# Kernel tuning notes

Measured on AMD Instinct MI355X. Metric: run time of the kernel, lower is better.

## Reference

```python
import jax, jax.numpy as jnp
import numpy as np

K = 20  # hard-coded in DGCNN.__init__

def _pd_neg(x):
    # negative squared pairwise distance, [B,N,C] -> [B,N,N]
    inner = jnp.einsum('bnc,bmc->bnm', x, x)
    sq = jnp.sum(x * x, axis=-1)
    return 2.0 * inner - sq[:, :, None] - sq[:, None, :]

def _knn(x):
    return jax.lax.top_k(_pd_neg(x), K)[1]  # [B,N,K]

def _edge_feat(x, idx):
    # x: [B,N,C], idx: [B,N,K] -> [B,N,K,2C] = concat(central, neighbor-central)
    nb = jax.vmap(lambda p, i: p[i])(x, idx)
    c = x[:, :, None, :]
    return jnp.concatenate([jnp.broadcast_to(c, nb.shape), nb - c], axis=-1)

def _conv(x, w, b, act=True):
    # 1x1 Conv2d == per-point linear; BN at inference with init stats is identity
    y = jnp.einsum('...c,cd->...d', x, w) + b
    return jax.nn.relu(y) if act else y

def _forward(x, tw1, tb1, tw2, tb2, tw3, tb3, tfw1, tfb1, tfw2, tfb2, txw, txb,
             e1w1, e1b1, e1w2, e1b2, e2w1, e2b1, e2w2, e2b2, e3w1, e3b1,
             c1w, c1b, c2w, c2b, c3w, c3b, c4w, c4b):
    pts = x[:, :, :3]
    # spatial transform net on edge features of raw xyz
    ef = _edge_feat(pts, _knn(pts))                      # [B,N,K,6]
    t = _conv(_conv(ef, tw1, tb1), tw2, tb2)
    t = jnp.max(t, axis=2)                               # max over neighbors
    t = _conv(t, tw3, tb3)                               # [B,N,1024]
    t = jnp.max(t, axis=1)                               # global maxpool -> [B,1024]
    t = jax.nn.relu(t @ tfw1 + tfb1)
    t = jax.nn.relu(t @ tfw2 + tfb2)
    xf = (t @ txw + txb).reshape(-1, 3, 3)
    p = jnp.einsum('bnc,bcd->bnd', pts, xf)              # transformed points
    # EdgeConv 1
    ef = _edge_feat(p, _knn(p))                          # [B,N,K,6]
    x1 = jnp.max(_conv(_conv(ef, e1w1, e1b1), e1w2, e1b2), axis=2)   # [B,N,64]
    # EdgeConv 2
    ef = _edge_feat(x1, _knn(x1))                        # [B,N,K,128]
    x2 = jnp.max(_conv(_conv(ef, e2w1, e2b1), e2w2, e2b2), axis=2)
    # EdgeConv 3
    ef = _edge_feat(x2, _knn(x2))
    x3 = jnp.max(_conv(ef, e3w1, e3b1), axis=2)
    # global feature + per-point head
    net = _conv(jnp.concatenate([x1, x2, x3], axis=-1), c1w, c1b)    # [B,N,1024]
    g = jnp.max(net, axis=1, keepdims=True)              # maxpool over all points
    g = jnp.broadcast_to(g, (g.shape[0], x1.shape[1], g.shape[2]))
    net = jnp.concatenate([g, x1, x2, x3], axis=-1)      # [B,N,1216]
    net = _conv(net, c2w, c2b)
    net = _conv(net, c3w, c3b)
    # dropout is identity at inference (training=False)
    return _conv(net, c4w, c4b, act=False)               # [B,N,num_classes]

def setup_inputs():
    keys = iter(jax.random.split(jax.random.key(0), 64))
    def w(*shape):
        return jax.random.normal(next(keys), shape, jnp.float32) / np.float32(np.sqrt(shape[0]))
    def b(n):
        return 0.01 * jax.random.normal(next(keys), (n,), jnp.float32)
    B, N, F = 4, 4096, 6
    d = dict(x=jax.random.normal(next(keys), (B, N, F), jnp.float32))
    d.update(tw1=w(6, 64), tb1=b(64), tw2=w(64, 128), tb2=b(128), tw3=w(128, 1024), tb3=b(1024),
             tfw1=w(1024, 512), tfb1=b(512), tfw2=w(512, 256), tfb2=b(256),
             txw=0.01 * w(256, 9), txb=jnp.eye(3, dtype=jnp.float32).reshape(9))
    d.update(e1w1=w(6, 64), e1b1=b(64), e1w2=w(64, 64), e1b2=b(64),
             e2w1=w(128, 64), e2b1=b(64), e2w2=w(64, 64), e2b2=b(64),
             e3w1=w(128, 64), e3b1=b(64))
    d.update(c1w=w(192, 1024), c1b=b(1024), c2w=w(1216, 512), c2b=b(512),
             c3w=w(512, 256), c3b=b(256), c4w=w(256, 2), c4b=b(2))
    return d

def reference(x, tw1, tb1, tw2, tb2, tw3, tb3, tfw1, tfb1, tfw2, tfb2, txw, txb,
              e1w1, e1b1, e1w2, e1b2, e2w1, e2b1, e2w2, e2b2, e3w1, e3b1,
              c1w, c1b, c2w, c2b, c3w, c3b, c4w, c4b):
    return _forward(x, tw1, tb1, tw2, tb2, tw3, tb3, tfw1, tfb1, tfw2, tfb2, txw, txb,
                    e1w1, e1b1, e1w2, e1b2, e2w1, e2b1, e2w2, e2b2, e3w1, e3b1,
                    c1w, c1b, c2w, c2b, c3w, c3b, c4w, c4b)
```

## Files before the change

kernel.cpp:

```cpp
#include <hip/hip_runtime.h>

#define Nn 4096
#define KK 20
#define BN 16384

typedef __attribute__((ext_vector_type(8))) short bf16x8;
typedef __attribute__((ext_vector_type(4))) float f32x4;

__device__ __forceinline__ unsigned short f2bf(float f) {
  unsigned int x = __float_as_uint(f);
  return (unsigned short)((x + 0x7fffu + ((x >> 16) & 1u)) >> 16);
}
__device__ __forceinline__ float bf2f(unsigned short u) {
  return __uint_as_float(((unsigned int)u) << 16);
}

__global__ void k_pts(const float* __restrict__ x, float* __restrict__ pts) {
  int i = blockIdx.x * 256 + threadIdx.x;
  if (i < BN * 3) {
    int pt = i / 3, c = i - 3 * pt;
    pts[i] = x[pt * 6 + c];
  }
}

__global__ void k_cvtT(const float* __restrict__ src, unsigned short* __restrict__ dst,
                       int N, int K, int ldn, int row0) {
  int i = blockIdx.x * 256 + threadIdx.x;
  if (i >= N * K) return;
  int n = i / K, k = i - n * K;
  dst[i] = f2bf(src[(size_t)(row0 + k) * ldn + n]);
}

__global__ void k_cvtT3(const float* __restrict__ src, unsigned short* __restrict__ h,
                        unsigned short* __restrict__ m, unsigned short* __restrict__ l,
                        int N, int K, int ldn) {
  int i = blockIdx.x * 256 + threadIdx.x;
  if (i >= N * K) return;
  int n = i / K, k = i - n * K;
  float x = src[(size_t)k * ldn + n];
  unsigned short hh = f2bf(x); float xh = bf2f(hh);
  unsigned short mm = f2bf(x - xh); float xm = bf2f(mm);
  unsigned short ll = f2bf(x - xh - xm);
  h[i] = hh; m[i] = mm; l[i] = ll;
}

__global__ void k_tv3(const float* __restrict__ part, const float* __restrict__ bias,
                      unsigned short* __restrict__ h, unsigned short* __restrict__ m,
                      unsigned short* __restrict__ l) {
  int i = blockIdx.x * 256 + threadIdx.x;
  if (i >= 16 * 1024) return;
  int row = i >> 10, col = i & 1023;
  float v = 0.f;
  if (row < 4) {
    float mx = -INFINITY;
#pragma unroll 8
    for (int s = 0; s < 32; ++s) mx = fmaxf(mx, part[((size_t)row * 32 + s) * 1024 + col]);
    v = fmaxf(mx + bias[col], 0.f);
  }
  unsigned short hh = f2bf(v); float xh = bf2f(hh);
  unsigned short mm = f2bf(v - xh); float xm = bf2f(mm);
  unsigned short ll = f2bf(v - xh - xm);
  h[i] = hh; m[i] = mm; l[i] = ll;
}

__global__ void k_pad3(const float* __restrict__ src, int rows, int cols,
                       unsigned short* __restrict__ h, unsigned short* __restrict__ m,
                       unsigned short* __restrict__ l) {
  int i = blockIdx.x * 256 + threadIdx.x;
  if (i >= 16 * cols) return;
  int row = i / cols, col = i - row * cols;
  float v = (row < rows) ? src[(size_t)row * cols + col] : 0.f;
  unsigned short hh = f2bf(v); float xh = bf2f(hh);
  unsigned short mm = f2bf(v - xh); float xm = bf2f(mm);
  unsigned short ll = f2bf(v - xh - xm);
  h[i] = hh; m[i] = mm; l[i] = ll;
}

template <int N, int K, int SEG>
__global__ __launch_bounds__(256) void k_gemmSK(const unsigned short* __restrict__ Ah,
                                                const unsigned short* __restrict__ Am,
                                                const unsigned short* __restrict__ Al,
                                                const unsigned short* __restrict__ Bh,
                                                const unsigned short* __restrict__ Bm,
                                                const unsigned short* __restrict__ Bl,
                                                float* __restrict__ partial) {
  constexpr int KSEG = K / SEG;
  constexpr int KS = KSEG / 32;
  int t = threadIdx.x;
  int wv = t >> 6, lane = t & 63;
  int quad = lane >> 4, l16 = lane & 15;
  int bx = blockIdx.x;
  int nb = bx / SEG, seg = bx - nb * SEG;
  int col = nb * 64 + wv * 16 + l16;
  int k0 = seg * KSEG;
  size_t wo = (size_t)col * K + k0 + quad * 8;
  size_t ao = (size_t)l16 * K + k0 + quad * 8;
  f32x4 acc = {0.f, 0.f, 0.f, 0.f};
#pragma unroll
  for (int s = 0; s < KS; ++s) {
    bf16x8 xh = *(const bf16x8*)(Ah + ao + s * 32);
    bf16x8 xm = *(const bf16x8*)(Am + ao + s * 32);
    bf16x8 xl = *(const bf16x8*)(Al + ao + s * 32);
    bf16x8 wh = *(const bf16x8*)(Bh + wo + s * 32);
    bf16x8 wm = *(const bf16x8*)(Bm + wo + s * 32);
    bf16x8 wl = *(const bf16x8*)(Bl + wo + s * 32);
    acc = __builtin_amdgcn_mfma_f32_16x16x32_bf16(xh, wh, acc, 0, 0, 0);
    acc = __builtin_amdgcn_mfma_f32_16x16x32_bf16(xh, wm, acc, 0, 0, 0);
    acc = __builtin_amdgcn_mfma_f32_16x16x32_bf16(xm, wh, acc, 0, 0, 0);
    acc = __builtin_amdgcn_mfma_f32_16x16x32_bf16(xh, wl, acc, 0, 0, 0);
    acc = __builtin_amdgcn_mfma_f32_16x16x32_bf16(xl, wh, acc, 0, 0, 0);
    acc = __builtin_amdgcn_mfma_f32_16x16x32_bf16(xm, wm, acc, 0, 0, 0);
  }
  if (quad == 0) {
#pragma unroll
    for (int r = 0; r < 4; ++r)
      partial[((size_t)seg * 4 + r) * N + col] = acc[r];
  }
}

__global__ void k_redS(const float* __restrict__ partial, const float* __restrict__ bias,
                       float* __restrict__ outp, int N, int SEG, int relu) {
  int i = blockIdx.x * 256 + threadIdx.x;
  if (i >= 4 * N) return;
  int r = i / N, c = i - r * N;
  float s = 0.f;
  for (int seg = 0; seg < SEG; ++seg) s += partial[((size_t)seg * 4 + r) * N + c];
  if (bias) s += bias[c];
  if (relu) s = fmaxf(s, 0.f);
  outp[(size_t)r * N + c] = s;
}

__global__ __launch_bounds__(256) void k_fc3p(const float* __restrict__ h2, const float* __restrict__ txw,
                                              const float* __restrict__ txb, const float* __restrict__ pts,
                                              float* __restrict__ p) {
  __shared__ float sh2[256];
  __shared__ float sxf[9];
  int t = threadIdx.x;
  int b = blockIdx.x;
  sh2[t] = h2[(size_t)b * 256 + t];
  __syncthreads();
  if (t < 9) {
    float acc = txb[t];
    for (int j = 0; j < 256; ++j) acc = fmaf(sh2[j], txw[j * 9 + t], acc);
    sxf[t] = acc;
  }
  __syncthreads();
  for (int n = t; n < Nn; n += 256) {
    const float* pr = pts + ((size_t)b * Nn + n) * 3;
    float a0 = pr[0], a1 = pr[1], a2 = pr[2];
    float* po = p + ((size_t)b * Nn + n) * 3;
#pragma unroll
    for (int d = 0; d < 3; ++d) po[d] = a0 * sxf[d] + a1 * sxf[3 + d] + a2 * sxf[6 + d];
  }
}

__device__ __forceinline__ float dist4(const float4* __restrict__ tile4, int c,
                                       float qx, float qy, float qz, float qsq) {
  float4 v = tile4[c];
  float dot = fmaf(qx, v.x, fmaf(qy, v.y, qz * v.z));
  return 2.0f * dot - qsq - v.w;
}

__global__ __launch_bounds__(1024) void k_knn3(const float* __restrict__ src, int* __restrict__ idx) {
  __shared__ float4 tile4[Nn];
  int t = threadIdx.x;
  int wave = t >> 6, lane = t & 63;
  int g = blockIdx.x * 16 + wave;
  int b = g >> 12, n = g & (Nn - 1);
  const float* base = src + (size_t)b * Nn * 3;
  for (int e = t; e < Nn; e += 1024) {
    float x = base[e * 3], y = base[e * 3 + 1], z = base[e * 3 + 2];
    tile4[e] = make_float4(x, y, z, fmaf(x, x, fmaf(y, y, z * z)));
  }
  __syncthreads();
  float4 q4 = tile4[n];
  float qx = q4.x, qy = q4.y, qz = q4.z, qsq = q4.w;
  float m1 = -INFINITY, m2 = -INFINITY, m3 = -INFINITY;
  int t1 = 0, t2 = 0, t3 = 0;
#pragma unroll 4
  for (int tt = 0; tt < 64; ++tt) {
    float dd = dist4(tile4, (tt << 6) + lane, qx, qy, qz, qsq);
    if (dd > m3) {
      if (dd > m1) { m3 = m2; t3 = t2; m2 = m1; t2 = t1; m1 = dd; t1 = tt; }
      else if (dd > m2) { m3 = m2; t3 = t2; m2 = dd; t2 = tt; }
      else { m3 = dd; t3 = tt; }
    }
  }
  unsigned long long removed = 0ull;
  int cnt = 3;
  int sel = 0;
#pragma unroll 1
  for (int k = 0; k < 20; ++k) {
    float v = m1; int ci = (t1 << 6) | lane;
    float mx = v;
#pragma unroll
    for (int off = 32; off; off >>= 1) mx = fmaxf(mx, __shfl_xor(mx, off, 64));
    int cand = (v == mx) ? ci : 0x7FFFFFFF;
#pragma unroll
    for (int off = 32; off; off >>= 1) cand = min(cand, __shfl_xor(cand, off, 64));
    if (k == lane) sel = cand;
    if (cand == ci) {
      removed |= 1ull << t1;
      if (cnt > 1) { m1 = m2; t1 = t2; m2 = m3; t2 = t3; --cnt; }
      else {
        m1 = -INFINITY; m2 = -INFINITY; m3 = -INFINITY; t1 = 0; t2 = 0; t3 = 0;
#pragma unroll 1
        for (int tt = 0; tt < 64; ++tt) {
          if ((removed >> tt) & 1ull) continue;
          float dd = dist4(tile4, (tt << 6) + lane, qx, qy, qz, qsq);
          if (dd > m3) {
            if (dd > m1) { m3 = m2; t3 = t2; m2 = m1; t2 = t1; m1 = dd; t1 = tt; }
            else if (dd > m2) { m3 = m2; t3 = t2; m2 = dd; t2 = tt; }
            else { m3 = dd; t3 = tt; }
          }
        }
        cnt = 3;
      }
    }
  }
  if (lane < 20) idx[(size_t)g * KK + lane] = sel;
}

__global__ void k_sqnorm(const float* __restrict__ src, float* __restrict__ out) {
  int g = blockIdx.x * 256 + threadIdx.x;
  if (g >= BN) return;
  const float4* r = (const float4*)(src + (size_t)g * 64);
  float s = 0.f;
#pragma unroll
  for (int j = 0; j < 16; ++j) { float4 v = r[j]; s += v.x * v.x + v.y * v.y + v.z * v.z + v.w * v.w; }
  out[g] = s;
}

__device__ __forceinline__ void topk_d3(const float (&d)[64], float m1, int t1, float m2, int t2,
                                        float m3, int t3, int lane, int* __restrict__ op) {
  unsigned long long removed = 0ull;
  int cnt = 3;
  int sel = 0;
#pragma unroll 1
  for (int k = 0; k < 20; ++k) {
    float v = m1; int ci = (t1 << 6) | lane;
    float mx = v;
#pragma unroll
    for (int off = 32; off; off >>= 1) mx = fmaxf(mx, __shfl_xor(mx, off, 64));
    int cand = (v == mx) ? ci : 0x7FFFFFFF;
#pragma unroll
    for (int off = 32; off; off >>= 1) cand = min(cand, __shfl_xor(cand, off, 64));
    if (k == lane) sel = cand;
    if (cand == ci) {
      removed |= 1ull << t1;
      if (cnt > 1) { m1 = m2; t1 = t2; m2 = m3; t2 = t3; --cnt; }
      else {
        m1 = -INFINITY; m2 = -INFINITY; m3 = -INFINITY; t1 = 0; t2 = 0; t3 = 0;
#pragma unroll
        for (int tt = 0; tt < 64; ++tt) {
          if (!((removed >> tt) & 1ull)) {
            float dv = d[tt];
            if (dv > m3) {
              if (dv > m1) { m3 = m2; t3 = t2; m2 = m1; t2 = t1; m1 = dv; t1 = tt; }
              else if (dv > m2) { m3 = m2; t3 = t2; m2 = dv; t2 = tt; }
              else { m3 = dv; t3 = tt; }
            }
          }
        }
        cnt = 3;
      }
    }
  }
  if (lane < 20) op[lane] = sel;
}

__global__ void __launch_bounds__(1024)
__attribute__((amdgpu_waves_per_eu(4, 4)))
k_dsel(const unsigned short* __restrict__ Xh,
       const unsigned short* __restrict__ Xm,
       const unsigned short* __restrict__ Xl,
       const float* __restrict__ sq,
       int* __restrict__ idx) {
  __shared__ float sD[16 * 1028];
  int t = threadIdx.x;
  int wave = t >> 6, lane = t & 63;
  int quad = lane >> 4, l16 = lane & 15;
  int blk = blockIdx.x;
  int b = blk >> 8, rs = blk & 255;
  int r0 = rs * 16;
  const size_t base = (size_t)b * Nn * 64;
  const float* sqb = sq + b * Nn;
  bf16x8 ah[2], am[2], al[2];
#pragma unroll
  for (int ks = 0; ks < 2; ++ks) {
    size_t ra = base + (size_t)(r0 + l16) * 64 + ks * 32 + quad * 8;
    ah[ks] = *(const bf16x8*)(Xh + ra);
    am[ks] = *(const bf16x8*)(Xm + ra);
    al[ks] = *(const bf16x8*)(Xl + ra);
  }
  float sqr[4];
#pragma unroll
  for (int r = 0; r < 4; ++r) sqr[r] = sqb[r0 + quad * 4 + r];
  float d[64];
  float m1 = -INFINITY, m2 = -INFINITY, m3 = -INFINITY;
  int t1 = 0, t2 = 0, t3 = 0;
#pragma unroll
  for (int ch = 0; ch < 4; ++ch) {
#pragma unroll
    for (int tt = 0; tt < 4; ++tt) {
      int cc = wave * 64 + tt * 16;
      int cb = ch * 1024 + cc;
      f32x4 acc = {0.f, 0.f, 0.f, 0.f};
#pragma unroll
      for (int ks = 0; ks < 2; ++ks) {
        size_t rb = base + (size_t)(cb + l16) * 64 + ks * 32 + quad * 8;
        bf16x8 bh = *(const bf16x8*)(Xh + rb);
        bf16x8 bm = *(const bf16x8*)(Xm + rb);
        bf16x8 bl = *(const bf16x8*)(Xl + rb);
        acc = __builtin_amdgcn_mfma_f32_16x16x32_bf16(ah[ks], bh, acc, 0, 0, 0);
        acc = __builtin_amdgcn_mfma_f32_16x16x32_bf16(ah[ks], bm, acc, 0, 0, 0);
        acc = __builtin_amdgcn_mfma_f32_16x16x32_bf16(am[ks], bh, acc, 0, 0, 0);
        acc = __builtin_amdgcn_mfma_f32_16x16x32_bf16(ah[ks], bl, acc, 0, 0, 0);
        acc = __builtin_amdgcn_mfma_f32_16x16x32_bf16(al[ks], bh, acc, 0, 0, 0);
        acc = __builtin_amdgcn_mfma_f32_16x16x32_bf16(am[ks], bm, acc, 0, 0, 0);
      }
      float sqc = sqb[cb + l16];
#pragma unroll
      for (int r = 0; r < 4; ++r)
        sD[(quad * 4 + r) * 1028 + cc + l16] = 2.0f * acc[r] - sqr[r] - sqc;
    }
    __syncthreads();
#pragma unroll
    for (int jj = 0; jj < 16; ++jj) {
      int tt = ch * 16 + jj;
      float dd = sD[wave * 1028 + jj * 64 + lane];
      d[tt] = dd;
      if (dd > m3) {
        if (dd > m1) { m3 = m2; t3 = t2; m2 = m1; t2 = t1; m1 = dd; t1 = tt; }
        else if (dd > m2) { m3 = m2; t3 = t2; m2 = dd; t2 = tt; }
        else { m3 = dd; t3 = tt; }
      }
    }
    __syncthreads();
  }
  topk_d3(d, m1, t1, m2, t2, m3, t3, lane, idx + (size_t)(b * Nn + r0 + wave) * KK);
}

__global__ __launch_bounds__(256) void k_uv3(const float* __restrict__ pts, const float* __restrict__ w1,
                                             const float* __restrict__ b1, float* __restrict__ uvb) {
  __shared__ float sw[384];
  __shared__ float sb[64];
  int t = threadIdx.x;
  for (int e = t; e < 384; e += 256) sw[e] = w1[e];
  if (t < 64) sb[t] = b1[t];
  __syncthreads();
  int pl = t >> 6, c = t & 63;
  int p = blockIdx.x * 4 + pl;
  const float* pr = pts + (size_t)p * 3;
  float x0 = pr[0], x1 = pr[1], x2 = pr[2];
  float wb0 = sw[192 + c], wb1 = sw[256 + c], wb2 = sw[320 + c];
  float v = x0 * wb0 + x1 * wb1 + x2 * wb2;
  float u = sb[c] + x0 * (sw[c] - wb0) + x1 * (sw[64 + c] - wb1) + x2 * (sw[128 + c] - wb2);
  uvb[(size_t)p * 128 + c] = u;
  uvb[(size_t)p * 128 + 64 + c] = v;
}

__global__ void k_prepD(const float* __restrict__ w1, float* __restrict__ Md) {
  int i = blockIdx.x * 256 + threadIdx.x;
  if (i >= 8192) return;
  int j = i >> 7, c = i & 127;
  Md[i] = (c < 64) ? (w1[j * 64 + c] - w1[(64 + j) * 64 + c]) : w1[(64 + j) * 64 + (c - 64)];
}

__global__ __launch_bounds__(256) void k_uv(const float* __restrict__ x2, const float* __restrict__ Md,
                                            const float* __restrict__ bias, float* __restrict__ uv) {
  __shared__ float sM[8192];
  __shared__ float sx[64 * 68];
  int t = threadIdx.x;
  for (int e = t; e < 8192; e += 256) sM[e] = Md[e];
  int p0 = blockIdx.x * 64;
  for (int e = t; e < 1024; e += 256) {
    int r = e >> 4, c4 = e & 15;
    *(float4*)(sx + r * 68 + c4 * 4) = *(const float4*)(x2 + (size_t)(p0 + r) * 64 + c4 * 4);
  }
  __syncthreads();
  int c = t & 127, rg = t >> 7;
  float badd = (c < 64) ? bias[c] : 0.f;
  float accv[32];
#pragma unroll
  for (int r = 0; r < 32; ++r) accv[r] = 0.f;
#pragma unroll
  for (int jc = 0; jc < 8; ++jc) {
    float mreg[8];
#pragma unroll
    for (int q = 0; q < 8; ++q) mreg[q] = sM[(jc * 8 + q) * 128 + c];
#pragma unroll
    for (int r = 0; r < 32; ++r) {
      const float* xr = sx + (rg * 32 + r) * 68 + jc * 8;
      float4 a = *(const float4*)xr, bb = *(const float4*)(xr + 4);
      float s = accv[r];
      s = fmaf(a.x, mreg[0], s); s = fmaf(a.y, mreg[1], s);
      s = fmaf(a.z, mreg[2], s); s = fmaf(a.w, mreg[3], s);
      s = fmaf(bb.x, mreg[4], s); s = fmaf(bb.y, mreg[5], s);
      s = fmaf(bb.z, mreg[6], s); s = fmaf(bb.w, mreg[7], s);
      accv[r] = s;
    }
  }
#pragma unroll
  for (int r = 0; r < 32; ++r)
    uv[(size_t)(p0 + rg * 32 + r) * 128 + c] = accv[r] + badd;
}

template <int NOUT, bool WRITEF, bool SPLIT3, bool CAT>
__global__ __launch_bounds__(256, 4) void k_econv(const float* __restrict__ uv,
                                                  const int* __restrict__ idx,
                                                  const unsigned short* __restrict__ W2h,
                                                  const unsigned short* __restrict__ W2m,
                                                  const unsigned short* __restrict__ W2l,
                                                  const float* __restrict__ b2,
                                                  float* __restrict__ outF,
                                                  unsigned short* __restrict__ oh,
                                                  unsigned short* __restrict__ om,
                                                  unsigned short* __restrict__ ol,
                                                  unsigned short* __restrict__ ocat,
                                                  int catoff) {
  __shared__ unsigned short y3[4][3][20 * 72];
  int t = threadIdx.x;
  int wv = t >> 6, lane = t & 63;
  int quad = lane >> 4, l16 = lane & 15;
  int p0 = blockIdx.x * 4;
  int p = p0 + wv;
  size_t nbase = (size_t)(p >> 12) * Nn;
  constexpr int CT = NOUT / 64;
  bf16x8 wfh[CT][2], wfm[CT][2], wfl[CT][2];
#pragma unroll
  for (int ct = 0; ct < CT; ++ct)
#pragma unroll
    for (int ks = 0; ks < 2; ++ks) {
      size_t wo = (size_t)(wv * (CT * 16) + ct * 16 + l16) * 64 + ks * 32 + quad * 8;
      wfh[ct][ks] = *(const bf16x8*)(W2h + wo);
      wfm[ct][ks] = *(const bf16x8*)(W2m + wo);
      wfl[ct][ks] = *(const bf16x8*)(W2l + wo);
    }
  const int* ip = idx + (size_t)p * KK;
  float u = uv[(size_t)p * 128 + lane];
  unsigned short* yh = y3[wv][0];
  unsigned short* ym = y3[wv][1];
  unsigned short* yl = y3[wv][2];
  float vv[20];
#pragma unroll
  for (int k = 0; k < 20; ++k) {
    int nb = ip[k];
    vv[k] = uv[(nbase + nb) * 128 + 64 + lane];
  }
#pragma unroll
  for (int k = 0; k < 20; ++k) {
    float y = fmaxf(u + vv[k], 0.f);
    unsigned short hh = f2bf(y); float fh = bf2f(hh);
    unsigned short mm = f2bf(y - fh); float fm = bf2f(mm);
    unsigned short ll = f2bf(y - fh - fm);
    yh[k * 72 + lane] = hh;
    ym[k * 72 + lane] = mm;
    yl[k * 72 + lane] = ll;
  }
  __syncthreads();
#pragma unroll 1
  for (int pp = 0; pp < 4; ++pp) {
    const unsigned short* ph0 = y3[pp][0];
    const unsigned short* pm0 = y3[pp][1];
    const unsigned short* pl0 = y3[pp][2];
    f32x4 acc[CT][2];
#pragma unroll
    for (int ct = 0; ct < CT; ++ct) {
      acc[ct][0] = (f32x4){0.f, 0.f, 0.f, 0.f};
      acc[ct][1] = (f32x4){0.f, 0.f, 0.f, 0.f};
    }
#pragma unroll
    for (int ks = 0; ks < 2; ++ks) {
      bf16x8 ah[2], am[2], al[2];
#pragma unroll
      for (int mt = 0; mt < 2; ++mt) {
        int row = mt * 16 + l16;
        int rr = (row < 20) ? row : 0;
        int aoff = rr * 72 + ks * 32 + quad * 8;
        ah[mt] = *(const bf16x8*)(ph0 + aoff);
        am[mt] = *(const bf16x8*)(pm0 + aoff);
        al[mt] = *(const bf16x8*)(pl0 + aoff);
      }
#pragma unroll
      for (int ct = 0; ct < CT; ++ct)
#pragma unroll
        for (int mt = 0; mt < 2; ++mt) {
          f32x4 a = acc[ct][mt];
          a = __builtin_amdgcn_mfma_f32_16x16x32_bf16(ah[mt], wfh[ct][ks], a, 0, 0, 0);
          a = __builtin_amdgcn_mfma_f32_16x16x32_bf16(ah[mt], wfm[ct][ks], a, 0, 0, 0);
          a = __builtin_amdgcn_mfma_f32_16x16x32_bf16(am[mt], wfh[ct][ks], a, 0, 0, 0);
          a = __builtin_amdgcn_mfma_f32_16x16x32_bf16(ah[mt], wfl[ct][ks], a, 0, 0, 0);
          a = __builtin_amdgcn_mfma_f32_16x16x32_bf16(al[mt], wfh[ct][ks], a, 0, 0, 0);
          a = __builtin_amdgcn_mfma_f32_16x16x32_bf16(am[mt], wfm[ct][ks], a, 0, 0, 0);
          acc[ct][mt] = a;
        }
    }
    int pt = p0 + pp;
#pragma unroll
    for (int ct = 0; ct < CT; ++ct) {
      int col = wv * (CT * 16) + ct * 16 + l16;
      float m0 = fmaxf(fmaxf(acc[ct][0][0], acc[ct][0][1]), fmaxf(acc[ct][0][2], acc[ct][0][3]));
      float m1v = (quad == 0)
                      ? fmaxf(fmaxf(acc[ct][1][0], acc[ct][1][1]), fmaxf(acc[ct][1][2], acc[ct][1][3]))
                      : -INFINITY;
      float m = fmaxf(m0, m1v);
      m = fmaxf(m, __shfl_xor(m, 16, 64));
      m = fmaxf(m, __shfl_xor(m, 32, 64));
      if (quad == 0) {
        float v = fmaxf(m + b2[col], 0.f);
        if (WRITEF) outF[(size_t)pt * NOUT + col] = v;
        if (SPLIT3) {
          unsigned short hh = f2bf(v); float fh = bf2f(hh);
          unsigned short mm2 = f2bf(v - fh); float fm = bf2f(mm2);
          unsigned short ll = f2bf(v - fh - fm);
          oh[(size_t)pt * NOUT + col] = hh;
          om[(size_t)pt * NOUT + col] = mm2;
          ol[(size_t)pt * NOUT + col] = ll;
        }
        if (CAT) ocat[(size_t)pt * 192 + catoff + col] = f2bf(v);
      }
    }
  }
}

__global__ __launch_bounds__(256) void k_gmax(const float* __restrict__ uv, const int* __restrict__ idx,
                                              unsigned short* __restrict__ ocat) {
  __shared__ int sidx[4][20];
  int t = threadIdx.x;
  int pl = t >> 6, c = t & 63;
  int p0 = blockIdx.x * 4;
  if (t < 80) sidx[t / 20][t % 20] = idx[(size_t)(p0 + t / 20) * KK + (t % 20)];
  __syncthreads();
  int p = p0 + pl;
  size_t nbase = (size_t)(p >> 12) * Nn;
  float u = uv[(size_t)p * 128 + c];
  float m = -INFINITY;
#pragma unroll
  for (int k = 0; k < 20; ++k) m = fmaxf(m, uv[(nbase + sidx[pl][k]) * 128 + 64 + c]);
  ocat[(size_t)p * 192 + 128 + c] = f2bf(fmaxf(u + m, 0.f));
}

template <int K>
__global__ __launch_bounds__(256) void k_mgemm(const unsigned short* __restrict__ A,
                                               const unsigned short* __restrict__ WT,
                                               float* __restrict__ outp) {
  constexpr int KS = K / 32;
  int t = threadIdx.x;
  int wv = t >> 6, lane = t & 63;
  int quad = lane >> 4, l16 = lane & 15;
  int blk = blockIdx.x;
  int b = blk >> 9, cb = (blk >> 5) & 15, ns = blk & 31;
  int n0 = cb * 64 + wv * 16;
  bf16x8 bfr[KS];
  const unsigned short* wrow = WT + (size_t)(n0 + l16) * K + quad * 8;
#pragma unroll
  for (int s = 0; s < KS; ++s) bfr[s] = *(const bf16x8*)(wrow + s * 32);
  const unsigned short* Ab = A + ((size_t)b * Nn + ns * 128 + l16) * K + quad * 8;
  float rmax = -INFINITY;
#pragma unroll 2
  for (int mt = 0; mt < 8; ++mt) {
    const unsigned short* ar = Ab + (size_t)mt * 16 * K;
    f32x4 acc = {0.f, 0.f, 0.f, 0.f};
#pragma unroll
    for (int s = 0; s < KS; ++s) {
      bf16x8 af = *(const bf16x8*)(ar + s * 32);
      acc = __builtin_amdgcn_mfma_f32_16x16x32_bf16(af, bfr[s], acc, 0, 0, 0);
    }
    rmax = fmaxf(rmax, fmaxf(fmaxf(acc[0], acc[1]), fmaxf(acc[2], acc[3])));
  }
  rmax = fmaxf(rmax, __shfl_xor(rmax, 16, 64));
  rmax = fmaxf(rmax, __shfl_xor(rmax, 32, 64));
  if (quad == 0) outp[((size_t)b * 32 + ns) * 1024 + n0 + l16] = rmax;
}

template <int K>
__global__ __launch_bounds__(256) void k_mgemm3s(const unsigned short* __restrict__ Ah,
                                                 const unsigned short* __restrict__ Am,
                                                 const unsigned short* __restrict__ Al,
                                                 const unsigned short* __restrict__ Bh,
                                                 const unsigned short* __restrict__ Bm,
                                                 const unsigned short* __restrict__ Bl,
                                                 float* __restrict__ outp) {
  constexpr int KS = K / 32;
  int t = threadIdx.x;
  int wv = t >> 6, lane = t & 63;
  int quad = lane >> 4, l16 = lane & 15;
  int blk = blockIdx.x;
  int b = blk >> 9, cb = (blk >> 5) & 15, ns = blk & 31;
  int n0 = cb * 64 + wv * 16;
  bf16x8 wh[KS], wm[KS], wl[KS];
  size_t wo = (size_t)(n0 + l16) * K + quad * 8;
#pragma unroll
  for (int s = 0; s < KS; ++s) {
    wh[s] = *(const bf16x8*)(Bh + wo + s * 32);
    wm[s] = *(const bf16x8*)(Bm + wo + s * 32);
    wl[s] = *(const bf16x8*)(Bl + wo + s * 32);
  }
  size_t ao = ((size_t)b * Nn + ns * 128 + l16) * K + quad * 8;
  float rmax = -INFINITY;
#pragma unroll 1
  for (int mt = 0; mt < 8; ++mt) {
    size_t ar = ao + (size_t)mt * 16 * K;
    f32x4 acc = {0.f, 0.f, 0.f, 0.f};
#pragma unroll
    for (int s = 0; s < KS; ++s) {
      bf16x8 xh = *(const bf16x8*)(Ah + ar + s * 32);
      bf16x8 xm = *(const bf16x8*)(Am + ar + s * 32);
      bf16x8 xl = *(const bf16x8*)(Al + ar + s * 32);
      acc = __builtin_amdgcn_mfma_f32_16x16x32_bf16(xh, wh[s], acc, 0, 0, 0);
      acc = __builtin_amdgcn_mfma_f32_16x16x32_bf16(xh, wm[s], acc, 0, 0, 0);
      acc = __builtin_amdgcn_mfma_f32_16x16x32_bf16(xm, wh[s], acc, 0, 0, 0);
      acc = __builtin_amdgcn_mfma_f32_16x16x32_bf16(xh, wl[s], acc, 0, 0, 0);
      acc = __builtin_amdgcn_mfma_f32_16x16x32_bf16(xl, wh[s], acc, 0, 0, 0);
      acc = __builtin_amdgcn_mfma_f32_16x16x32_bf16(xm, wm[s], acc, 0, 0, 0);
    }
    rmax = fmaxf(rmax, fmaxf(fmaxf(acc[0], acc[1]), fmaxf(acc[2], acc[3])));
  }
  rmax = fmaxf(rmax, __shfl_xor(rmax, 16, 64));
  rmax = fmaxf(rmax, __shfl_xor(rmax, 32, 64));
  if (quad == 0) outp[((size_t)b * 32 + ns) * 1024 + n0 + l16] = rmax;
}

__global__ __launch_bounds__(256) void k_final(const unsigned short* __restrict__ xcat,
                                               const float* __restrict__ gc,
                                               const float* __restrict__ c2b,
                                               const unsigned short* __restrict__ c2wT,
                                               const unsigned short* __restrict__ c3wT,
                                               const float* __restrict__ c3b,
                                               const float* __restrict__ c4w, const float* __restrict__ c4b,
                                               float* __restrict__ out) {
  __shared__ unsigned short z5[16 * 520];
  __shared__ float z2[16 * 260];
  int t = threadIdx.x;
  int wv = t >> 6, lane = t & 63;
  int quad = lane >> 4, l16 = lane & 15;
  int p0 = blockIdx.x * 16;
  int b = p0 >> 12;
  bf16x8 a1[6];
  const unsigned short* ar = xcat + (size_t)(p0 + l16) * 192 + quad * 8;
#pragma unroll
  for (int s = 0; s < 6; ++s) a1[s] = *(const bf16x8*)(ar + s * 32);
#pragma unroll 1
  for (int ntw = 0; ntw < 8; ++ntw) {
    int col = wv * 128 + ntw * 16 + l16;
    float bias = gc[(size_t)b * 512 + col] + c2b[col];
    f32x4 acc = {bias, bias, bias, bias};
    const unsigned short* wr = c2wT + (size_t)col * 192 + quad * 8;
#pragma unroll
    for (int s = 0; s < 6; ++s) {
      bf16x8 bfr = *(const bf16x8*)(wr + s * 32);
      acc = __builtin_amdgcn_mfma_f32_16x16x32_bf16(a1[s], bfr, acc, 0, 0, 0);
    }
#pragma unroll
    for (int r = 0; r < 4; ++r)
      z5[(quad * 4 + r) * 520 + col] = f2bf(fmaxf(acc[r], 0.f));
  }
  __syncthreads();
  bf16x8 a2[16];
#pragma unroll
  for (int s = 0; s < 16; ++s) a2[s] = *(const bf16x8*)(z5 + l16 * 520 + s * 32 + quad * 8);
#pragma unroll 1
  for (int ntw = 0; ntw < 4; ++ntw) {
    int col = wv * 64 + ntw * 16 + l16;
    float bias = c3b[col];
    f32x4 acc = {bias, bias, bias, bias};
    const unsigned short* wr = c3wT + (size_t)col * 512 + quad * 8;
#pragma unroll
    for (int s = 0; s < 16; ++s) {
      bf16x8 bfr = *(const bf16x8*)(wr + s * 32);
      acc = __builtin_amdgcn_mfma_f32_16x16x32_bf16(a2[s], bfr, acc, 0, 0, 0);
    }
#pragma unroll
    for (int r = 0; r < 4; ++r)
      z2[(quad * 4 + r) * 260 + col] = fmaxf(acc[r], 0.f);
  }
  __syncthreads();
  if (t < 32) {
    int m = t >> 1, e = t & 1;
    float acc = c4b[e];
    const float* zr = z2 + m * 260;
    for (int j = 0; j < 256; ++j) acc = fmaf(zr[j], c4w[j * 2 + e], acc);
    out[(size_t)(p0 + m) * 2 + e] = acc;
  }
}

extern "C" void kernel_launch(void* const* d_in, const int* in_sizes, int n_in,
                              void* d_out, int out_size, void* d_ws, size_t ws_size,
                              hipStream_t stream) {
  const float* xin = (const float*)d_in[0];
  const float* W[30];
  for (int i = 0; i < 30; ++i) W[i] = (const float*)d_in[i + 1];

  float* ws = (float*)d_ws;
  size_t off = 0;
  float* pts   = ws + off; off += (size_t)BN * 3;
  float* p     = ws + off; off += (size_t)BN * 3;
  int*   idx   = (int*)(ws + off); off += (size_t)BN * KK;
  float* sq    = ws + off; off += BN;
  float* dpart = ws + off; off += 4 * 32 * 1024;
  float* h1    = ws + off; off += 4 * 512;
  float* h2b   = ws + off; off += 4 * 256;
  float* x1    = ws + off; off += (size_t)BN * 64;
  float* x2    = ws + off; off += (size_t)BN * 64;
  float* gpart = ws + off; off += 4 * 32 * 1024;
  float* gc    = ws + off; off += 4 * 512;
  float* uvb   = ws + off; off += (size_t)BN * 128;
  float* partial = ws + off; off += 16 * 4 * 512;
  unsigned short* xcat = (unsigned short*)(ws + off); off += (size_t)BN * 96;
  unsigned short* c1wT = (unsigned short*)(ws + off); off += 98304;
  unsigned short* c2wT = (unsigned short*)(ws + off); off += 49152;
  unsigned short* c3wT = (unsigned short*)(ws + off); off += 65536;
  unsigned short* w3Th = (unsigned short*)(ws + off); off += 65536;
  unsigned short* w3Tm = (unsigned short*)(ws + off); off += 65536;
  unsigned short* w3Tl = (unsigned short*)(ws + off); off += 65536;
  unsigned short* tw2h = (unsigned short*)(ws + off); off += 4096;
  unsigned short* tw2m = (unsigned short*)(ws + off); off += 4096;
  unsigned short* tw2l = (unsigned short*)(ws + off); off += 4096;
  unsigned short* e1h  = (unsigned short*)(ws + off); off += 2048;
  unsigned short* e1m  = (unsigned short*)(ws + off); off += 2048;
  unsigned short* e1l  = (unsigned short*)(ws + off); off += 2048;
  unsigned short* e2h  = (unsigned short*)(ws + off); off += 2048;
  unsigned short* e2m  = (unsigned short*)(ws + off); off += 2048;
  unsigned short* e2l  = (unsigned short*)(ws + off); off += 2048;
  unsigned short* xsh  = (unsigned short*)(ws + off); off += 524288;
  unsigned short* xsm  = (unsigned short*)(ws + off); off += 524288;
  unsigned short* xsl  = (unsigned short*)(ws + off); off += 524288;
  float* MdC   = ws + off; off += 8192;
  float* MdD   = ws + off; off += 8192;
  unsigned short* fw1h = (unsigned short*)(ws + off); off += 262144;
  unsigned short* fw1m = (unsigned short*)(ws + off); off += 262144;
  unsigned short* fw1l = (unsigned short*)(ws + off); off += 262144;
  unsigned short* cw2h = (unsigned short*)(ws + off); off += 262144;
  unsigned short* cw2m = (unsigned short*)(ws + off); off += 262144;
  unsigned short* cw2l = (unsigned short*)(ws + off); off += 262144;
  unsigned short* fw2h = (unsigned short*)(ws + off); off += 65536;
  unsigned short* fw2m = (unsigned short*)(ws + off); off += 65536;
  unsigned short* fw2l = (unsigned short*)(ws + off); off += 65536;
  unsigned short* tvh  = (unsigned short*)(ws + off); off += 8192;
  unsigned short* tvm  = (unsigned short*)(ws + off); off += 8192;
  unsigned short* tvl  = (unsigned short*)(ws + off); off += 8192;
  unsigned short* h13h = (unsigned short*)(ws + off); off += 4096;
  unsigned short* h13m = (unsigned short*)(ws + off); off += 4096;
  unsigned short* h13l = (unsigned short*)(ws + off); off += 4096;
  float* Dbuf  = ws + off; off += (size_t)Nn * Nn;
  unsigned short* t3h = (unsigned short*)Dbuf;
  unsigned short* t3m = t3h + (size_t)BN * 128;
  unsigned short* t3l = t3m + (size_t)BN * 128;

  k_cvtT<<<dim3(768), dim3(256), 0, stream>>>(W[22], c1wT, 1024, 192, 1024, 0);
  k_cvtT<<<dim3(384), dim3(256), 0, stream>>>(W[24], c2wT, 512, 192, 512, 1024);
  k_cvtT<<<dim3(512), dim3(256), 0, stream>>>(W[26], c3wT, 256, 512, 256, 0);
  k_cvtT3<<<dim3(512), dim3(256), 0, stream>>>(W[4], w3Th, w3Tm, w3Tl, 1024, 128, 1024);
  k_cvtT3<<<dim3(32), dim3(256), 0, stream>>>(W[2], tw2h, tw2m, tw2l, 128, 64, 128);
  k_cvtT3<<<dim3(16), dim3(256), 0, stream>>>(W[14], e1h, e1m, e1l, 64, 64, 64);
  k_cvtT3<<<dim3(16), dim3(256), 0, stream>>>(W[18], e2h, e2m, e2l, 64, 64, 64);
  k_cvtT3<<<dim3(2048), dim3(256), 0, stream>>>(W[6], fw1h, fw1m, fw1l, 512, 1024, 512);
  k_cvtT3<<<dim3(2048), dim3(256), 0, stream>>>(W[24], cw2h, cw2m, cw2l, 512, 1024, 512);
  k_cvtT3<<<dim3(512), dim3(256), 0, stream>>>(W[8], fw2h, fw2m, fw2l, 256, 512, 256);
  k_prepD<<<dim3(32), dim3(256), 0, stream>>>(W[16], MdC);
  k_prepD<<<dim3(32), dim3(256), 0, stream>>>(W[20], MdD);

  k_pts<<<dim3(192), dim3(256), 0, stream>>>(xin, pts);

  k_knn3<<<dim3(1024), dim3(1024), 0, stream>>>(pts, idx);
  k_uv3<<<dim3(4096), dim3(256), 0, stream>>>(pts, W[0], W[1], uvb);
  k_econv<128, false, true, false><<<dim3(4096), dim3(256), 0, stream>>>(
      uvb, idx, tw2h, tw2m, tw2l, W[3], nullptr, t3h, t3m, t3l, nullptr, 0);
  k_mgemm3s<128><<<dim3(2048), dim3(256), 0, stream>>>(t3h, t3m, t3l, w3Th, w3Tm, w3Tl, dpart);
  k_tv3<<<dim3(64), dim3(256), 0, stream>>>(dpart, W[5], tvh, tvm, tvl);
  k_gemmSK<512, 1024, 16><<<dim3(128), dim3(256), 0, stream>>>(tvh, tvm, tvl, fw1h, fw1m, fw1l, partial);
  k_redS<<<dim3(8), dim3(256), 0, stream>>>(partial, W[7], h1, 512, 16, 1);
  k_pad3<<<dim3(32), dim3(256), 0, stream>>>(h1, 4, 512, h13h, h13m, h13l);
  k_gemmSK<256, 512, 8><<<dim3(32), dim3(256), 0, stream>>>(h13h, h13m, h13l, fw2h, fw2m, fw2l, partial);
  k_redS<<<dim3(4), dim3(256), 0, stream>>>(partial, W[9], h2b, 256, 8, 1);
  k_fc3p<<<dim3(4), dim3(256), 0, stream>>>(h2b, W[10], W[11], pts, p);

  k_knn3<<<dim3(1024), dim3(1024), 0, stream>>>(p, idx);
  k_uv3<<<dim3(4096), dim3(256), 0, stream>>>(p, W[12], W[13], uvb);
  k_econv<64, true, true, true><<<dim3(4096), dim3(256), 0, stream>>>(
      uvb, idx, e1h, e1m, e1l, W[15], x1, xsh, xsm, xsl, xcat, 0);
  k_sqnorm<<<dim3(64), dim3(256), 0, stream>>>(x1, sq);
  k_dsel<<<dim3(1024), dim3(1024), 0, stream>>>(xsh, xsm, xsl, sq, idx);
  k_uv<<<dim3(256), dim3(256), 0, stream>>>(x1, MdC, W[17], uvb);
  k_econv<64, true, true, true><<<dim3(4096), dim3(256), 0, stream>>>(
      uvb, idx, e2h, e2m, e2l, W[19], x2, xsh, xsm, xsl, xcat, 64);
  k_sqnorm<<<dim3(64), dim3(256), 0, stream>>>(x2, sq);
  k_dsel<<<dim3(1024), dim3(1024), 0, stream>>>(xsh, xsm, xsl, sq, idx);
  k_uv<<<dim3(256), dim3(256), 0, stream>>>(x2, MdD, W[21], uvb);
  k_gmax<<<dim3(4096), dim3(256), 0, stream>>>(uvb, idx, xcat);

  k_mgemm<192><<<dim3(2048), dim3(256), 0, stream>>>(xcat, c1wT, gpart);
  k_tv3<<<dim3(64), dim3(256), 0, stream>>>(gpart, W[23], tvh, tvm, tvl);
  k_gemmSK<512, 1024, 16><<<dim3(128), dim3(256), 0, stream>>>(tvh, tvm, tvl, cw2h, cw2m, cw2l, partial);
  k_redS<<<dim3(8), dim3(256), 0, stream>>>(partial, nullptr, gc, 512, 16, 0);
  k_final<<<dim3(1024), dim3(256), 0, stream>>>(xcat, gc, W[25], c2wT, c3wT,
                                                W[27], W[28], W[29], (float*)d_out);
}
```

Baseline: 1.282 ms.

## Spill kNN distance rows to a global buffer and launch per batch

The per-lane 64-element distance array in the kNN select kernel is replaced with a global scratch buffer, and the top-k refill scan now rereads distances from memory. The launch is split into four per-batch launches so the scratch buffer covers one batch at a time. The aim is to cut register pressure and raise occupancy. In exchange it adds global write and reread traffic for the full distance matrix, plus extra launches.

```diff
diff --git a/kernel.cpp b/kernel.cpp
--- a/kernel.cpp
+++ b/kernel.cpp
@@ -231,8 +231,8 @@
   out[g] = s;
 }
 
-__device__ __forceinline__ void topk_d3(const float (&d)[64], float m1, int t1, float m2, int t2,
-                                        float m3, int t3, int lane, int* __restrict__ op) {
+__device__ __forceinline__ void topk_g(const float* __restrict__ Drow, float m1, int t1, float m2, int t2,
+                                       float m3, int t3, int lane, int* __restrict__ op) {
   unsigned long long removed = 0ull;
   int cnt = 3;
   int sel = 0;
@@ -251,15 +251,13 @@
       if (cnt > 1) { m1 = m2; t1 = t2; m2 = m3; t2 = t3; --cnt; }
       else {
         m1 = -INFINITY; m2 = -INFINITY; m3 = -INFINITY; t1 = 0; t2 = 0; t3 = 0;
-#pragma unroll
+#pragma unroll 8
         for (int tt = 0; tt < 64; ++tt) {
-          if (!((removed >> tt) & 1ull)) {
-            float dv = d[tt];
-            if (dv > m3) {
-              if (dv > m1) { m3 = m2; t3 = t2; m2 = m1; t2 = t1; m1 = dv; t1 = tt; }
-              else if (dv > m2) { m3 = m2; t3 = t2; m2 = dv; t2 = tt; }
-              else { m3 = dv; t3 = tt; }
-            }
+          float dv = Drow[(tt << 6) | lane];
+          if (!((removed >> tt) & 1ull) && dv > m3) {
+            if (dv > m1) { m3 = m2; t3 = t2; m2 = m1; t2 = t1; m1 = dv; t1 = tt; }
+            else if (dv > m2) { m3 = m2; t3 = t2; m2 = dv; t2 = tt; }
+            else { m3 = dv; t3 = tt; }
           }
         }
         cnt = 3;
@@ -269,20 +267,17 @@
   if (lane < 20) op[lane] = sel;
 }
 
-__global__ void __launch_bounds__(1024)
-__attribute__((amdgpu_waves_per_eu(4, 4)))
-k_dsel(const unsigned short* __restrict__ Xh,
-       const unsigned short* __restrict__ Xm,
-       const unsigned short* __restrict__ Xl,
-       const float* __restrict__ sq,
-       int* __restrict__ idx) {
+__global__ __launch_bounds__(1024) void k_dsel(const unsigned short* __restrict__ Xh,
+                                               const unsigned short* __restrict__ Xm,
+                                               const unsigned short* __restrict__ Xl,
+                                               const float* __restrict__ sq,
+                                               int b, float* __restrict__ Dg,
+                                               int* __restrict__ idx) {
   __shared__ float sD[16 * 1028];
   int t = threadIdx.x;
   int wave = t >> 6, lane = t & 63;
   int quad = lane >> 4, l16 = lane & 15;
-  int blk = blockIdx.x;
-  int b = blk >> 8, rs = blk & 255;
-  int r0 = rs * 16;
+  int r0 = blockIdx.x * 16;
   const size_t base = (size_t)b * Nn * 64;
   const float* sqb = sq + b * Nn;
   bf16x8 ah[2], am[2], al[2];
@@ -296,7 +291,7 @@
   float sqr[4];
 #pragma unroll
   for (int r = 0; r < 4; ++r) sqr[r] = sqb[r0 + quad * 4 + r];
-  float d[64];
+  float* Drow = Dg + (size_t)(r0 + wave) * 4096;
   float m1 = -INFINITY, m2 = -INFINITY, m3 = -INFINITY;
   int t1 = 0, t2 = 0, t3 = 0;
 #pragma unroll
@@ -329,7 +324,7 @@
     for (int jj = 0; jj < 16; ++jj) {
       int tt = ch * 16 + jj;
       float dd = sD[wave * 1028 + jj * 64 + lane];
-      d[tt] = dd;
+      Drow[(tt << 6) | lane] = dd;
       if (dd > m3) {
         if (dd > m1) { m3 = m2; t3 = t2; m2 = m1; t2 = t1; m1 = dd; t1 = tt; }
         else if (dd > m2) { m3 = m2; t3 = t2; m2 = dd; t2 = tt; }
@@ -338,7 +333,7 @@
     }
     __syncthreads();
   }
-  topk_d3(d, m1, t1, m2, t2, m3, t3, lane, idx + (size_t)(b * Nn + r0 + wave) * KK);
+  topk_g(Drow, m1, t1, m2, t2, m3, t3, lane, idx + (size_t)(b * Nn + r0 + wave) * KK);
 }
 
 __global__ __launch_bounds__(256) void k_uv3(const float* __restrict__ pts, const float* __restrict__ w1,
@@ -781,12 +776,14 @@
   k_econv<64, true, true, true><<<dim3(4096), dim3(256), 0, stream>>>(
       uvb, idx, e1h, e1m, e1l, W[15], x1, xsh, xsm, xsl, xcat, 0);
   k_sqnorm<<<dim3(64), dim3(256), 0, stream>>>(x1, sq);
-  k_dsel<<<dim3(1024), dim3(1024), 0, stream>>>(xsh, xsm, xsl, sq, idx);
+  for (int b = 0; b < 4; ++b)
+    k_dsel<<<dim3(256), dim3(1024), 0, stream>>>(xsh, xsm, xsl, sq, b, Dbuf, idx);
   k_uv<<<dim3(256), dim3(256), 0, stream>>>(x1, MdC, W[17], uvb);
   k_econv<64, true, true, true><<<dim3(4096), dim3(256), 0, stream>>>(
       uvb, idx, e2h, e2m, e2l, W[19], x2, xsh, xsm, xsl, xcat, 64);
   k_sqnorm<<<dim3(64), dim3(256), 0, stream>>>(x2, sq);
-  k_dsel<<<dim3(1024), dim3(1024), 0, stream>>>(xsh, xsm, xsl, sq, idx);
+  for (int b = 0; b < 4; ++b)
+    k_dsel<<<dim3(256), dim3(1024), 0, stream>>>(xsh, xsm, xsl, sq, b, Dbuf, idx);
   k_uv<<<dim3(256), dim3(256), 0, stream>>>(x2, MdD, W[21], uvb);
   k_gmax<<<dim3(4096), dim3(256), 0, stream>>>(uvb, idx, xcat);
 
```

Result: slower. 1.564 ms (+22.0%).
